# Kernel tuning notes

Measured on AMD Instinct MI355X. Metric: run time of the kernel, lower is better.

Reference implementation:

```python
import jax, jax.numpy as jnp
import numpy as np

T, B, D = 2048, 16, 1024

def setup_inputs() -> dict:
    key = jax.random.key(0)
    k1, k2 = jax.random.split(key)
    x = jax.random.normal(k1, (T, B, D), dtype=jnp.float32)
    # xavier-uniform init for W (dim, dim)
    limit = float(np.sqrt(6.0 / (D + D)))
    W = jax.random.uniform(k2, (D, D), dtype=jnp.float32, minval=-limit, maxval=limit)
    b = jnp.zeros((D,), dtype=jnp.float32)
    return {"x": x, "W": W, "b": b}

def reference(x, W, b):
    Tn, Bn, Dn = x.shape
    h0 = jnp.zeros((Bn, Dn), dtype=x.dtype)
    # parallel projection: v_t = W @ x_t + b for all t
    proj_all = jnp.einsum('tbd,ed->tbe', x, W) + b  # [T, B, D]

    def step(h_prev, proj):
        alpha = jax.nn.sigmoid(proj)
        h_new = alpha * h_prev + (1.0 - alpha) * jnp.tanh(proj)
        out = h_new * jax.nn.silu(h_new)  # h * silu(h)
        return h_new, (h_new, out)

    _, (hs, outputs) = jax.lax.scan(step, h0, proj_all)
    h = jnp.concatenate([h0[None], hs], axis=0)  # [T+1, B, D]
    return (outputs, h)
```

## Files before the change

### kernel.cpp

```cpp
#include <hip/hip_runtime.h>

#define T_DIM 2048
#define B_DIM 16
#define D_DIM 1024
#define M_DIM (T_DIM * B_DIM)
#define K_DIM D_DIM
#define N_DIM D_DIM
#define BD    (B_DIM * D_DIM)
#define NCH   32
#define CHL   (T_DIM / NCH)
#define NQ    (BD / 4)

typedef _Float16 f16;
typedef __attribute__((ext_vector_type(8)))  _Float16 f16x8;
typedef __attribute__((ext_vector_type(4)))  float    f32x4;

#define GLD16(g, l) __builtin_amdgcn_global_load_lds(                        \
    (const __attribute__((address_space(1))) unsigned*)(g),                  \
    (__attribute__((address_space(3))) unsigned*)(l), 16, 0, 0)

#define CFENCE asm volatile("" ::: "memory")
#define BARRIER do { CFENCE; __builtin_amdgcn_s_barrier(); CFENCE; } while (0)

__device__ __forceinline__ void stepAB(float p, float& A, float& B) {
    const float ep  = __expf(-p);
    const float al  = __builtin_amdgcn_rcpf(1.f + ep);
    const float be  = ep * al;
    const float ep2 = ep * ep;
    const float th  = (1.f - ep2) * __builtin_amdgcn_rcpf(1.f + ep2);
    A = A * al;
    B = fmaf(al, B, be * th);
}
__device__ __forceinline__ void stepH(float p, float& h) {
    const float ep  = __expf(-p);
    const float al  = __builtin_amdgcn_rcpf(1.f + ep);
    const float be  = ep * al;
    const float ep2 = ep * ep;
    const float th  = (1.f - ep2) * __builtin_amdgcn_rcpf(1.f + ep2);
    h = fmaf(al, h, be * th);
}
__device__ __forceinline__ float outOf(float h) {
    const float sh = __builtin_amdgcn_rcpf(1.f + __expf(-h));
    return h * h * sh;
}


__global__ __launch_bounds__(256) void convert_x(const float* __restrict__ x,
                                                 ushort* __restrict__ Xf) {
    __shared__ ushort tile[8192];
    const int b   = (int)blockIdx.x;
    const int br  = b >> 4;
    const int kt  = b & 15;
    const int tid = (int)threadIdx.x;
#pragma unroll
    for (int i = 0; i < 8; ++i) {
        const int fi  = tid + i * 256;
        const int row = fi >> 4;
        const int kq  = fi & 15;
        const float4 v = *(const float4*)&x[(size_t)(br * 128 + row) * K_DIM + kt * 64 + kq * 4];
        ushort4 u;
        u.x = __builtin_bit_cast(unsigned short, (f16)v.x);
        u.y = __builtin_bit_cast(unsigned short, (f16)v.y);
        u.z = __builtin_bit_cast(unsigned short, (f16)v.z);
        u.w = __builtin_bit_cast(unsigned short, (f16)v.w);
        const int idx = ((kq >> 1) * 128 + row) * 8 + (kq & 1) * 4;
        *(ushort4*)&tile[idx] = u;
    }
    __syncthreads();
    const uint4* s = (const uint4*)tile;
    uint4* d = (uint4*)(Xf + (size_t)b * 8192);
#pragma unroll
    for (int i = 0; i < 4; ++i) d[tid + i * 256] = s[tid + i * 256];
}

__global__ __launch_bounds__(256) void convert_w(const float* __restrict__ W,
                                                 ushort* __restrict__ Wh) {
    __shared__ ushort th[8192];
    const int b   = (int)blockIdx.x;
    const int bc  = b >> 4;
    const int kt  = b & 15;
    const int tid = (int)threadIdx.x;
#pragma unroll
    for (int i = 0; i < 8; ++i) {
        const int fi  = tid + i * 256;
        const int col = fi >> 4;
        const int kq  = fi & 15;
        const float4 v = *(const float4*)&W[(size_t)(bc * 128 + col) * K_DIM + kt * 64 + kq * 4];
        ushort4 u;
        u.x = __builtin_bit_cast(unsigned short, (f16)v.x);
        u.y = __builtin_bit_cast(unsigned short, (f16)v.y);
        u.z = __builtin_bit_cast(unsigned short, (f16)v.z);
        u.w = __builtin_bit_cast(unsigned short, (f16)v.w);
        const int idx = ((kq >> 1) * 128 + col) * 8 + (kq & 1) * 4;
        *(ushort4*)&th[idx] = u;
    }
    __syncthreads();
    const uint4* s = (const uint4*)th;
    uint4* d = (uint4*)(Wh + (size_t)b * 8192);
#pragma unroll
    for (int i = 0; i < 4; ++i) d[tid + i * 256] = s[tid + i * 256];
}

template <int OUT16>
__global__ __launch_bounds__(256, 2) void gemm_proj(const ushort* __restrict__ Xf,
                                                    const ushort* __restrict__ Wh,
                                                    const float* __restrict__ bias,
                                                    float* __restrict__ proj32,
                                                    ushort* __restrict__ proj16) {
    __shared__ ushort sA[2][8192];
    __shared__ ushort sB[2][8192];

    const int bid = (int)blockIdx.x;
    const int swz = (bid & 7) * 256 + (bid >> 3);
    const int bc  = swz & 7;
    const int br  = swz >> 3;
    const int tid  = (int)threadIdx.x;
    const int lane = tid & 63;
    const int wid  = tid >> 6;
    const int wr = (wid >> 1) * 64;
    const int wc = (wid & 1) * 64;
    const int l16 = lane & 15;
    const int lc  = lane >> 4;

    const char* aG = (const char*)(Xf + (size_t)br * 16 * 8192);
    const char* bG = (const char*)(Wh + (size_t)bc * 16 * 8192);

    f32x4 acc[4][4];
#pragma unroll
    for (int m = 0; m < 4; ++m)
#pragma unroll
        for (int n = 0; n < 4; ++n)
#pragma unroll
            for (int r = 0; r < 4; ++r) acc[m][n][r] = 0.f;

#define STAGE(t, buf) do {                                                   \
        const size_t tb = (size_t)(t) * 16384;                               \
        GLD16(aG + tb + tid * 16,         (char*)&sA[buf][0] + tid * 16);    \
        GLD16(aG + tb + tid * 16 + 4096,  (char*)&sA[buf][0] + tid * 16 + 4096);  \
        GLD16(aG + tb + tid * 16 + 8192,  (char*)&sA[buf][0] + tid * 16 + 8192);  \
        GLD16(aG + tb + tid * 16 + 12288, (char*)&sA[buf][0] + tid * 16 + 12288); \
        GLD16(bG + tb + tid * 16,         (char*)&sB[buf][0] + tid * 16);    \
        GLD16(bG + tb + tid * 16 + 4096,  (char*)&sB[buf][0] + tid * 16 + 4096);  \
        GLD16(bG + tb + tid * 16 + 8192,  (char*)&sB[buf][0] + tid * 16 + 8192);  \
        GLD16(bG + tb + tid * 16 + 12288, (char*)&sB[buf][0] + tid * 16 + 12288); \
    } while (0)

    STAGE(0, 0);
    STAGE(1, 1);

    for (int t = 0; t < 16; ++t) {
        if (t < 15) asm volatile("s_waitcnt vmcnt(8)" ::: "memory");
        else        asm volatile("s_waitcnt vmcnt(0)" ::: "memory");
        BARRIER;
        const int cur = t & 1;
#pragma unroll
        for (int kc = 0; kc < 2; ++kc) {
            const int cbase = (kc * 4 + lc) * 128;
            f16x8 fa[4], fb[4];
#pragma unroll
            for (int m = 0; m < 4; ++m)
                fa[m] = *(const f16x8*)&sA[cur][(cbase + wr + m * 16 + l16) * 8];
#pragma unroll
            for (int n = 0; n < 4; ++n)
                fb[n] = *(const f16x8*)&sB[cur][(cbase + wc + n * 16 + l16) * 8];
#pragma unroll
            for (int m = 0; m < 4; ++m)
#pragma unroll
                for (int n = 0; n < 4; ++n)
                    acc[m][n] = __builtin_amdgcn_mfma_f32_16x16x32_f16(fa[m], fb[n], acc[m][n], 0, 0, 0);
        }
        BARRIER;
        if (t < 14) STAGE(t + 2, cur);
    }
#undef STAGE

#pragma unroll
    for (int n = 0; n < 4; ++n) {
        const int colg = bc * 128 + wc + n * 16 + l16;
        const float bz = bias[colg];
#pragma unroll
        for (int m = 0; m < 4; ++m) {
            const int rowg = br * 128 + wr + m * 16 + lc * 4;
#pragma unroll
            for (int r = 0; r < 4; ++r) {
                const float v = acc[m][n][r] + bz;
                if constexpr (OUT16)
                    proj16[(size_t)(rowg + r) * N_DIM + colg] =
                        __builtin_bit_cast(unsigned short, (f16)v);
                else
                    proj32[(size_t)(rowg + r) * N_DIM + colg] = v;
            }
        }
    }
}

__global__ __launch_bounds__(256) void scan_pass1h(const ushort* __restrict__ po,
                                                   float* __restrict__ Ac,
                                                   float* __restrict__ Bc) {
    const int blk = (int)blockIdx.x;
    const int c   = blk >> 3;
    const int q   = (blk & 7) * 256 + (int)threadIdx.x;
    const ushort* pp = po + (size_t)c * CHL * BD + (size_t)q * 8;

    float A[8], B[8];
#pragma unroll
    for (int e = 0; e < 8; ++e) { A[e] = 1.f; B[e] = 0.f; }

    f16x8 cur[4], nxt[4];
#pragma unroll
    for (int j = 0; j < 4; ++j) cur[j] = *(const f16x8*)&pp[(size_t)j * BD];
    for (int g = 0; g < CHL / 4; ++g) {
        if (g + 1 < CHL / 4) {
#pragma unroll
            for (int j = 0; j < 4; ++j)
                nxt[j] = *(const f16x8*)&pp[(size_t)((g + 1) * 4 + j) * BD];
        }
#pragma unroll
        for (int j = 0; j < 4; ++j)
#pragma unroll
            for (int e = 0; e < 8; ++e)
                stepAB((float)cur[j][e], A[e], B[e]);
#pragma unroll
        for (int j = 0; j < 4; ++j) cur[j] = nxt[j];
    }
    float* ap = Ac + (size_t)c * BD + (size_t)q * 8;
    float* bp = Bc + (size_t)c * BD + (size_t)q * 8;
    *(float4*)&ap[0] = make_float4(A[0], A[1], A[2], A[3]);
    *(float4*)&ap[4] = make_float4(A[4], A[5], A[6], A[7]);
    *(float4*)&bp[0] = make_float4(B[0], B[1], B[2], B[3]);
    *(float4*)&bp[4] = make_float4(B[4], B[5], B[6], B[7]);
}

__global__ __launch_bounds__(256) void scan_pass2h(const ushort* __restrict__ po,
                                                   const float* __restrict__ Ac,
                                                   const float* __restrict__ Bc,
                                                   float* __restrict__ out,
                                                   float* __restrict__ h_out) {
    const int blk = (int)blockIdx.x;
    const int c   = blk >> 3;
    const int q   = (blk & 7) * 256 + (int)threadIdx.x;

    float h[8];
#pragma unroll
    for (int e = 0; e < 8; ++e) h[e] = 0.f;
    for (int j = 0; j < c; ++j) {
        const float* ap = Ac + (size_t)j * BD + (size_t)q * 8;
        const float* bp = Bc + (size_t)j * BD + (size_t)q * 8;
        const float4 a0 = *(const float4*)&ap[0], a1 = *(const float4*)&ap[4];
        const float4 b0 = *(const float4*)&bp[0], b1 = *(const float4*)&bp[4];
        h[0] = fmaf(a0.x, h[0], b0.x); h[1] = fmaf(a0.y, h[1], b0.y);
        h[2] = fmaf(a0.z, h[2], b0.z); h[3] = fmaf(a0.w, h[3], b0.w);
        h[4] = fmaf(a1.x, h[4], b1.x); h[5] = fmaf(a1.y, h[5], b1.y);
        h[6] = fmaf(a1.z, h[6], b1.z); h[7] = fmaf(a1.w, h[7], b1.w);
    }
    if (c == 0) {
        *(float4*)&h_out[(size_t)q * 8]     = make_float4(0.f, 0.f, 0.f, 0.f);
        *(float4*)&h_out[(size_t)q * 8 + 4] = make_float4(0.f, 0.f, 0.f, 0.f);
    }

    const ushort* pp = po + (size_t)c * CHL * BD + (size_t)q * 8;
    float* op = out   + (size_t)c * CHL * BD + (size_t)q * 8;
    float* hp = h_out + (size_t)c * CHL * BD + (size_t)q * 8 + BD;

    f16x8 cur[4], nxt[4];
#pragma unroll
    for (int j = 0; j < 4; ++j) cur[j] = *(const f16x8*)&pp[(size_t)j * BD];
    for (int g = 0; g < CHL / 4; ++g) {
        if (g + 1 < CHL / 4) {
#pragma unroll
            for (int j = 0; j < 4; ++j)
                nxt[j] = *(const f16x8*)&pp[(size_t)((g + 1) * 4 + j) * BD];
        }
#pragma unroll
        for (int j = 0; j < 4; ++j) {
            const size_t so = (size_t)(g * 4 + j) * BD;
            float o[8];
#pragma unroll
            for (int e = 0; e < 8; ++e) {
                stepH((float)cur[j][e], h[e]);
                o[e] = outOf(h[e]);
            }
            *(float4*)&op[so]     = make_float4(o[0], o[1], o[2], o[3]);
            *(float4*)&op[so + 4] = make_float4(o[4], o[5], o[6], o[7]);
            *(float4*)&hp[so]     = make_float4(h[0], h[1], h[2], h[3]);
            *(float4*)&hp[so + 4] = make_float4(h[4], h[5], h[6], h[7]);
        }
#pragma unroll
        for (int j = 0; j < 4; ++j) cur[j] = nxt[j];
    }
}

__global__ __launch_bounds__(256) void scan_pass1(const float* __restrict__ po,
                                                  float4* __restrict__ Ac,
                                                  float4* __restrict__ Bc) {
    const int blk = (int)blockIdx.x;
    const int c   = blk >> 4;
    const int q   = (blk & 15) * 256 + (int)threadIdx.x;
    const float* pp = po + (size_t)c * CHL * BD + (size_t)q * 4;

    float4 A = make_float4(1.f, 1.f, 1.f, 1.f);
    float4 B = make_float4(0.f, 0.f, 0.f, 0.f);
    float4 cur[4], nxt[4];
#pragma unroll
    for (int j = 0; j < 4; ++j) cur[j] = *(const float4*)&pp[(size_t)j * BD];
    for (int g = 0; g < CHL / 4; ++g) {
        if (g + 1 < CHL / 4) {
#pragma unroll
            for (int j = 0; j < 4; ++j)
                nxt[j] = *(const float4*)&pp[(size_t)((g + 1) * 4 + j) * BD];
        }
#pragma unroll
        for (int j = 0; j < 4; ++j) {
            stepAB(cur[j].x, A.x, B.x);
            stepAB(cur[j].y, A.y, B.y);
            stepAB(cur[j].z, A.z, B.z);
            stepAB(cur[j].w, A.w, B.w);
        }
#pragma unroll
        for (int j = 0; j < 4; ++j) cur[j] = nxt[j];
    }
    Ac[c * NQ + q] = A;
    Bc[c * NQ + q] = B;
}

__global__ __launch_bounds__(256) void scan_pass2(float* __restrict__ po,
                                                  const float4* __restrict__ Ac,
                                                  const float4* __restrict__ Bc,
                                                  float* __restrict__ h_out) {
    const int blk = (int)blockIdx.x;
    const int c   = blk >> 4;
    const int q   = (blk & 15) * 256 + (int)threadIdx.x;

    float4 h = make_float4(0.f, 0.f, 0.f, 0.f);
    for (int j = 0; j < c; ++j) {
        const float4 A = Ac[j * NQ + q];
        const float4 B = Bc[j * NQ + q];
        h.x = fmaf(A.x, h.x, B.x);
        h.y = fmaf(A.y, h.y, B.y);
        h.z = fmaf(A.z, h.z, B.z);
        h.w = fmaf(A.w, h.w, B.w);
    }
    if (c == 0) *(float4*)&h_out[(size_t)q * 4] = make_float4(0.f, 0.f, 0.f, 0.f);

    float* pp = po + (size_t)c * CHL * BD + (size_t)q * 4;
    float* hp = h_out + (size_t)c * CHL * BD + (size_t)q * 4 + BD;

    float4 cur[4], nxt[4];
#pragma unroll
    for (int j = 0; j < 4; ++j) cur[j] = *(const float4*)&pp[(size_t)j * BD];
    for (int g = 0; g < CHL / 4; ++g) {
        if (g + 1 < CHL / 4) {
#pragma unroll
            for (int j = 0; j < 4; ++j)
                nxt[j] = *(const float4*)&pp[(size_t)((g + 1) * 4 + j) * BD];
        }
#pragma unroll
        for (int j = 0; j < 4; ++j) {
            const size_t so = (size_t)(g * 4 + j) * BD;
            stepH(cur[j].x, h.x);
            stepH(cur[j].y, h.y);
            stepH(cur[j].z, h.z);
            stepH(cur[j].w, h.w);
            float4 o;
            o.x = outOf(h.x); o.y = outOf(h.y); o.z = outOf(h.z); o.w = outOf(h.w);
            *(float4*)&pp[so] = o;
            *(float4*)&hp[so] = h;
        }
#pragma unroll
        for (int j = 0; j < 4; ++j) cur[j] = nxt[j];
    }
}

__global__ __launch_bounds__(64) void scan_fused(float* __restrict__ po,
                                                 float* __restrict__ h_out) {
    const int idx = (int)blockIdx.x * 64 + (int)threadIdx.x;
    float h = 0.f;
    h_out[idx] = 0.f;
    size_t off = (size_t)idx;
#pragma unroll 4
    for (int t = 0; t < T_DIM; ++t) {
        float p = po[off];
        stepH(p, h);
        po[off] = outOf(h);
        h_out[off + BD] = h;
        off += BD;
    }
}

extern "C" void kernel_launch(void* const* d_in, const int* in_sizes, int n_in,
                              void* d_out, int out_size, void* d_ws, size_t ws_size,
                              hipStream_t stream) {
    const float* x = (const float*)d_in[0];
    const float* W = (const float*)d_in[1];
    const float* b = (const float*)d_in[2];
    float* out = (float*)d_out;
    float* h   = out + (size_t)T_DIM * B_DIM * D_DIM;

    ushort* Xf = (ushort*)h;
    ushort* Wh = Xf + (size_t)M_DIM * K_DIM;

    convert_x<<<4096, 256, 0, stream>>>(x, Xf);
    convert_w<<<128, 256, 0, stream>>>(W, Wh);

    const size_t P16_BYTES = (size_t)M_DIM * N_DIM * 2;
    const size_t AB_BYTES  = (size_t)NCH * BD * 4;

    if (ws_size >= P16_BYTES + 2 * AB_BYTES) {
        ushort* P16 = (ushort*)d_ws;
        float*  Ac  = (float*)((char*)d_ws + P16_BYTES);
        float*  Bc  = Ac + (size_t)NCH * BD;
        gemm_proj<1><<<2048, 256, 0, stream>>>(Xf, Wh, b, nullptr, P16);
        scan_pass1h<<<(NCH - 1) * 8, 256, 0, stream>>>(P16, Ac, Bc);
        scan_pass2h<<<NCH * 8, 256, 0, stream>>>(P16, Ac, Bc, out, h);
    } else if (ws_size >= (size_t)4 * 1024 * 1024) {
        float4* Ac = (float4*)d_ws;
        float4* Bc = Ac + (size_t)NCH * NQ;
        gemm_proj<0><<<2048, 256, 0, stream>>>(Xf, Wh, b, out, nullptr);
        scan_pass1<<<(NCH - 1) * 16, 256, 0, stream>>>(out, Ac, Bc);
        scan_pass2<<<NCH * 16, 256, 0, stream>>>(out, Ac, Bc, h);
    } else {
        gemm_proj<0><<<2048, 256, 0, stream>>>(Xf, Wh, b, out, nullptr);
        scan_fused<<<BD / 64, 64, 0, stream>>>(out, h);
    }
}
```

Before: 213.8 us.

## Fuse fp32-to-fp16 conversion of x into the projection GEMM

```diff
diff --git a/kernel.cpp b/kernel.cpp
--- a/kernel.cpp
+++ b/kernel.cpp
@@ -19,9 +19,6 @@
     (const __attribute__((address_space(1))) unsigned*)(g),                  \
     (__attribute__((address_space(3))) unsigned*)(l), 16, 0, 0)
 
-#define CFENCE asm volatile("" ::: "memory")
-#define BARRIER do { CFENCE; __builtin_amdgcn_s_barrier(); CFENCE; } while (0)
-
 __device__ __forceinline__ void stepAB(float p, float& A, float& B) {
     const float ep  = __expf(-p);
     const float al  = __builtin_amdgcn_rcpf(1.f + ep);
@@ -44,34 +41,6 @@
     return h * h * sh;
 }
 
-
-__global__ __launch_bounds__(256) void convert_x(const float* __restrict__ x,
-                                                 ushort* __restrict__ Xf) {
-    __shared__ ushort tile[8192];
-    const int b   = (int)blockIdx.x;
-    const int br  = b >> 4;
-    const int kt  = b & 15;
-    const int tid = (int)threadIdx.x;
-#pragma unroll
-    for (int i = 0; i < 8; ++i) {
-        const int fi  = tid + i * 256;
-        const int row = fi >> 4;
-        const int kq  = fi & 15;
-        const float4 v = *(const float4*)&x[(size_t)(br * 128 + row) * K_DIM + kt * 64 + kq * 4];
-        ushort4 u;
-        u.x = __builtin_bit_cast(unsigned short, (f16)v.x);
-        u.y = __builtin_bit_cast(unsigned short, (f16)v.y);
-        u.z = __builtin_bit_cast(unsigned short, (f16)v.z);
-        u.w = __builtin_bit_cast(unsigned short, (f16)v.w);
-        const int idx = ((kq >> 1) * 128 + row) * 8 + (kq & 1) * 4;
-        *(ushort4*)&tile[idx] = u;
-    }
-    __syncthreads();
-    const uint4* s = (const uint4*)tile;
-    uint4* d = (uint4*)(Xf + (size_t)b * 8192);
-#pragma unroll
-    for (int i = 0; i < 4; ++i) d[tid + i * 256] = s[tid + i * 256];
-}
 
 __global__ __launch_bounds__(256) void convert_w(const float* __restrict__ W,
                                                  ushort* __restrict__ Wh) {
@@ -102,11 +71,11 @@
 }
 
 template <int OUT16>
-__global__ __launch_bounds__(256, 2) void gemm_proj(const ushort* __restrict__ Xf,
-                                                    const ushort* __restrict__ Wh,
-                                                    const float* __restrict__ bias,
-                                                    float* __restrict__ proj32,
-                                                    ushort* __restrict__ proj16) {
+__global__ __launch_bounds__(256, 2) void gemm_fused(const float* __restrict__ x,
+                                                     const ushort* __restrict__ Wh,
+                                                     const float* __restrict__ bias,
+                                                     float* __restrict__ proj32,
+                                                     ushort* __restrict__ proj16) {
     __shared__ ushort sA[2][8192];
     __shared__ ushort sB[2][8192];
 
@@ -122,8 +91,19 @@
     const int l16 = lane & 15;
     const int lc  = lane >> 4;
 
-    const char* aG = (const char*)(Xf + (size_t)br * 16 * 8192);
-    const char* bG = (const char*)(Wh + (size_t)bc * 16 * 8192);
+    const float* xg = x + (size_t)(br * 128) * K_DIM;
+    const char*  bG = (const char*)(Wh + (size_t)bc * 16 * 8192);
+
+    size_t goff[4];
+    int    loff[4];
+#pragma unroll
+    for (int i = 0; i < 4; ++i) {
+        const int lin = tid + i * 256;
+        const int c   = lin >> 7;
+        const int row = lin & 127;
+        goff[i] = (size_t)row * K_DIM + c * 8;
+        loff[i] = lin * 8;
+    }
 
     f32x4 acc[4][4];
 #pragma unroll
@@ -133,26 +113,56 @@
 #pragma unroll
             for (int r = 0; r < 4; ++r) acc[m][n][r] = 0.f;
 
-#define STAGE(t, buf) do {                                                   \
-        const size_t tb = (size_t)(t) * 16384;                               \
-        GLD16(aG + tb + tid * 16,         (char*)&sA[buf][0] + tid * 16);    \
-        GLD16(aG + tb + tid * 16 + 4096,  (char*)&sA[buf][0] + tid * 16 + 4096);  \
-        GLD16(aG + tb + tid * 16 + 8192,  (char*)&sA[buf][0] + tid * 16 + 8192);  \
-        GLD16(aG + tb + tid * 16 + 12288, (char*)&sA[buf][0] + tid * 16 + 12288); \
-        GLD16(bG + tb + tid * 16,         (char*)&sB[buf][0] + tid * 16);    \
+    float4 ra[4], rb[4];
+
+#define ISSUE_A(t) do {                                                       \
+        const size_t ko = (size_t)(t) * 64;                                   \
+        ra[0] = *(const float4*)&xg[goff[0] + ko];                            \
+        rb[0] = *(const float4*)&xg[goff[0] + ko + 4];                        \
+        ra[1] = *(const float4*)&xg[goff[1] + ko];                            \
+        rb[1] = *(const float4*)&xg[goff[1] + ko + 4];                        \
+        ra[2] = *(const float4*)&xg[goff[2] + ko];                            \
+        rb[2] = *(const float4*)&xg[goff[2] + ko + 4];                        \
+        ra[3] = *(const float4*)&xg[goff[3] + ko];                            \
+        rb[3] = *(const float4*)&xg[goff[3] + ko + 4];                        \
+    } while (0)
+
+#define ISSUE_B(t, buf) do {                                                  \
+        const size_t tb = (size_t)(t) * 16384;                                \
+        GLD16(bG + tb + tid * 16,         (char*)&sB[buf][0] + tid * 16);     \
         GLD16(bG + tb + tid * 16 + 4096,  (char*)&sB[buf][0] + tid * 16 + 4096);  \
         GLD16(bG + tb + tid * 16 + 8192,  (char*)&sB[buf][0] + tid * 16 + 8192);  \
         GLD16(bG + tb + tid * 16 + 12288, (char*)&sB[buf][0] + tid * 16 + 12288); \
     } while (0)
 
-    STAGE(0, 0);
-    STAGE(1, 1);
+#define CVT_WRITE(buf) do {                                                   \
+        _Pragma("unroll")                                                     \
+        for (int i = 0; i < 4; ++i) {                                         \
+            union { ushort u[8]; uint4 q; } pk;                               \
+            pk.u[0] = __builtin_bit_cast(unsigned short, (f16)ra[i].x);       \
+            pk.u[1] = __builtin_bit_cast(unsigned short, (f16)ra[i].y);       \
+            pk.u[2] = __builtin_bit_cast(unsigned short, (f16)ra[i].z);       \
+            pk.u[3] = __builtin_bit_cast(unsigned short, (f16)ra[i].w);       \
+            pk.u[4] = __builtin_bit_cast(unsigned short, (f16)rb[i].x);       \
+            pk.u[5] = __builtin_bit_cast(unsigned short, (f16)rb[i].y);       \
+            pk.u[6] = __builtin_bit_cast(unsigned short, (f16)rb[i].z);       \
+            pk.u[7] = __builtin_bit_cast(unsigned short, (f16)rb[i].w);       \
+            *(uint4*)&sA[buf][loff[i]] = pk.q;                                \
+        }                                                                     \
+    } while (0)
+
+    ISSUE_A(0);
+    ISSUE_B(0, 0);
+    CVT_WRITE(0);
+    asm volatile("s_waitcnt vmcnt(0)" ::: "memory");
+    __syncthreads();
 
     for (int t = 0; t < 16; ++t) {
-        if (t < 15) asm volatile("s_waitcnt vmcnt(8)" ::: "memory");
-        else        asm volatile("s_waitcnt vmcnt(0)" ::: "memory");
-        BARRIER;
         const int cur = t & 1;
+        if (t < 15) {
+            ISSUE_A(t + 1);
+            ISSUE_B(t + 1, cur ^ 1);
+        }
 #pragma unroll
         for (int kc = 0; kc < 2; ++kc) {
             const int cbase = (kc * 4 + lc) * 128;
@@ -169,10 +179,15 @@
                 for (int n = 0; n < 4; ++n)
                     acc[m][n] = __builtin_amdgcn_mfma_f32_16x16x32_f16(fa[m], fb[n], acc[m][n], 0, 0, 0);
         }
-        BARRIER;
-        if (t < 14) STAGE(t + 2, cur);
-    }
-#undef STAGE
+        if (t < 15) {
+            CVT_WRITE(cur ^ 1);
+            asm volatile("s_waitcnt vmcnt(0)" ::: "memory");
+        }
+        __syncthreads();
+    }
+#undef ISSUE_A
+#undef ISSUE_B
+#undef CVT_WRITE
 
 #pragma unroll
     for (int n = 0; n < 4; ++n) {
@@ -396,10 +411,8 @@
     float* out = (float*)d_out;
     float* h   = out + (size_t)T_DIM * B_DIM * D_DIM;
 
-    ushort* Xf = (ushort*)h;
-    ushort* Wh = Xf + (size_t)M_DIM * K_DIM;
-
-    convert_x<<<4096, 256, 0, stream>>>(x, Xf);
+    ushort* Wh = (ushort*)h;
+
     convert_w<<<128, 256, 0, stream>>>(W, Wh);
 
     const size_t P16_BYTES = (size_t)M_DIM * N_DIM * 2;
@@ -409,17 +422,17 @@
         ushort* P16 = (ushort*)d_ws;
         float*  Ac  = (float*)((char*)d_ws + P16_BYTES);
         float*  Bc  = Ac + (size_t)NCH * BD;
-        gemm_proj<1><<<2048, 256, 0, stream>>>(Xf, Wh, b, nullptr, P16);
+        gemm_fused<1><<<2048, 256, 0, stream>>>(x, Wh, b, nullptr, P16);
         scan_pass1h<<<(NCH - 1) * 8, 256, 0, stream>>>(P16, Ac, Bc);
         scan_pass2h<<<NCH * 8, 256, 0, stream>>>(P16, Ac, Bc, out, h);
     } else if (ws_size >= (size_t)4 * 1024 * 1024) {
         float4* Ac = (float4*)d_ws;
         float4* Bc = Ac + (size_t)NCH * NQ;
-        gemm_proj<0><<<2048, 256, 0, stream>>>(Xf, Wh, b, out, nullptr);
+        gemm_fused<0><<<2048, 256, 0, stream>>>(x, Wh, b, out, nullptr);
         scan_pass1<<<(NCH - 1) * 16, 256, 0, stream>>>(out, Ac, Bc);
         scan_pass2<<<NCH * 16, 256, 0, stream>>>(out, Ac, Bc, h);
     } else {
-        gemm_proj<0><<<2048, 256, 0, stream>>>(Xf, Wh, b, out, nullptr);
+        gemm_fused<0><<<2048, 256, 0, stream>>>(x, Wh, b, out, nullptr);
         scan_fused<<<BD / 64, 64, 0, stream>>>(out, h);
     }
 }
```

Result: slower. 343.8 us (+60.8%).
